# Kernel tuning notes

Hardware: AMD Instinct MI355X
Metric: run time of the kernel (lower is better)

Reference implementation:

```python
import jax, jax.numpy as jnp
import numpy as np

B, N, F, K = 16384, 64, 128, 64


def setup_inputs() -> dict:
    key = jax.random.key(0)
    kx, kd = jax.random.split(key)
    x = jax.random.normal(kx, (B, F), dtype=jnp.float32)
    D = jax.random.normal(kd, (N, F, K), dtype=jnp.float32)  # per-cluster factor dictionaries
    return {"x": x, "D": D}


def reference(x, D):
    # --- assignment step (torch.no_grad in original) ---
    # Dtx[n,b,j] = sum_i D[n,i,j] * x[b,i]
    Dtx = jnp.einsum('nij,bi->nbj', D, x)                      # [N,B,K]
    # per-cluster (D^T D)^{-1}, batched inverse over the cluster axis
    DTD = jnp.einsum('nij,nik->njk', D, D)                     # [N,K,K]
    DTD_inv = jnp.linalg.inv(DTD)                              # [N,K,K]
    Cs = jnp.einsum('nbj,nkj->nbk', Dtx, DTD_inv)              # [N,B,K]
    x_hat = jnp.einsum('nij,nbj->nbi', D, Cs)                  # [N,B,F]
    # nearest-subspace assignment per sample
    label = jnp.argmin(jnp.linalg.norm(x_hat - x[None], axis=-1), axis=0)  # [B] int
    C = Cs[label, jnp.arange(x.shape[0])]                      # [B,K] gather per sample
    # --- reconstruction loss: sum_i || x[i] - D[label[i]] @ C[i] ||^2 ---
    x_rec = jnp.einsum('bik,bk->bi', D[label], C)              # grouped gather + matmul
    se_loss = jnp.sum(jnp.square(x - x_rec))
    return se_loss, label
```

## Files before the change

kernel.cpp:

```cpp
#include <hip/hip_runtime.h>
#include <hip/hip_bf16.h>

#define B_N 16384
#define TAU 0.25f
#define GS 68
#define YS 133

typedef float f32x4 __attribute__((ext_vector_type(4)));
typedef short s16x8 __attribute__((ext_vector_type(8)));

__device__ __forceinline__ void gl_lds16(const void* g, void* l) {
    __builtin_amdgcn_global_load_lds(
        (const __attribute__((address_space(1))) void*)g,
        (__attribute__((address_space(3))) void*)l, 16, 0, 0);
}

__device__ __forceinline__ unsigned short bf16_bits(float v) {
    __hip_bfloat16 h = __float2bfloat16(v);
    return *reinterpret_cast<unsigned short*>(&h);
}

__device__ __forceinline__ float readlane_f(float v, int l) {
    return __int_as_float(__builtin_amdgcn_readlane(__float_as_int(v), l));
}

__global__ __launch_bounds__(256) void prep_convert(const float* __restrict__ x,
                                                    const float* __restrict__ D,
                                                    unsigned short* __restrict__ xh,
                                                    float* __restrict__ nrm,
                                                    float* __restrict__ Qg,
                                                    unsigned short* __restrict__ Bht,
                                                    float* __restrict__ out) {
    const int t = threadIdx.x;

    if (blockIdx.x >= 64) {
        const int gid = (blockIdx.x - 64) * 256 + t;
        if (gid == 0) out[0] = 0.0f;
        const size_t base = (size_t)gid * 32;
        float s = 0.0f;
        #pragma unroll
        for (int c = 0; c < 8; ++c) {
            const f32x4 v = ((const f32x4*)(x + base))[c];
            s += v.x * v.x + v.y * v.y + v.z * v.z + v.w * v.w;
            ushort4 h;
            h.x = bf16_bits(v.x); h.y = bf16_bits(v.y);
            h.z = bf16_bits(v.z); h.w = bf16_bits(v.w);
            ((ushort4*)(xh + base))[c] = h;
        }
        s += __shfl_xor(s, 1, 64);
        s += __shfl_xor(s, 2, 64);
        if ((gid & 3) == 0) nrm[gid >> 2] = s;
        return;
    }

    __shared__ float Y[64 * YS];
    __shared__ __align__(16) float G[64 * GS + 64];
    __shared__ __align__(16) float Lti[8 * 8 * 8];
    const int n = blockIdx.x;
    const float* Dn = D + (size_t)n * 8192;

    for (int e4 = t; e4 < 2048; e4 += 256) {
        const int c = e4 >> 4, j4 = (e4 & 15) * 4;
        const f32x4 v = ((const f32x4*)Dn)[e4];
        Y[(j4 + 0) * YS + c] = v.x;
        Y[(j4 + 1) * YS + c] = v.y;
        Y[(j4 + 2) * YS + c] = v.z;
        Y[(j4 + 3) * YS + c] = v.w;
    }

    {
        const int a0 = (t & 15) * 4, b0 = (t >> 4) * 4;
        float acc[4][4] = {};
        #pragma unroll 4
        for (int i = 0; i < 128; ++i) {
            const f32x4 av = *(const f32x4*)(Dn + i * 64 + a0);
            const f32x4 bv = *(const f32x4*)(Dn + i * 64 + b0);
            const float aa[4] = {av.x, av.y, av.z, av.w};
            const float bb[4] = {bv.x, bv.y, bv.z, bv.w};
            #pragma unroll
            for (int p = 0; p < 4; ++p)
                #pragma unroll
                for (int q = 0; q < 4; ++q) acc[p][q] = fmaf(aa[p], bb[q], acc[p][q]);
        }
        #pragma unroll
        for (int p = 0; p < 4; ++p)
            #pragma unroll
            for (int q = 0; q < 4; ++q) G[(a0 + p) * GS + b0 + q] = acc[p][q];
    }
    __syncthreads();

    #pragma unroll
    for (int p8 = 0; p8 < 8; ++p8) {
        const int pb = p8 * 8;
        if (t < 64) {
            const int lane = t;
            const f32x4 v0 = *(const f32x4*)&G[lane * GS + pb];
            const f32x4 v1 = *(const f32x4*)&G[lane * GS + pb + 4];
            float g[8] = {v0.x, v0.y, v0.z, v0.w, v1.x, v1.y, v1.z, v1.w};
            #pragma unroll
            for (int kk = 0; kk < 8; ++kk) {
                const int k = pb + kk;
                const float dk = readlane_f(g[kk], k);
                const float rinv = 1.0f / sqrtf(dk);
                const float lik = g[kk] * rinv;
                g[kk] = lik;
                if (lane == 0) G[64 * GS + k] = rinv;
                #pragma unroll
                for (int jj = kk + 1; jj < 8; ++jj) {
                    const float ljk = readlane_f(lik, pb + jj);
                    g[jj] -= lik * ljk;
                }
            }
            *(f32x4*)&G[lane * GS + pb]     = (f32x4){g[0], g[1], g[2], g[3]};
            *(f32x4*)&G[lane * GS + pb + 4] = (f32x4){g[4], g[5], g[6], g[7]};
        }
        __syncthreads();
        const int base = pb + 8;
        if (base < 64) {
            for (int i = base + (t >> 5); i < 64; i += 8) {
                const f32x4 Li0 = *(const f32x4*)&G[i * GS + pb];
                const f32x4 Li1 = *(const f32x4*)&G[i * GS + pb + 4];
                for (int j = base + (t & 31); j < 64; j += 32) {
                    const f32x4 Lj0 = *(const f32x4*)&G[j * GS + pb];
                    const f32x4 Lj1 = *(const f32x4*)&G[j * GS + pb + 4];
                    float s = G[i * GS + j];
                    s -= Li0.x * Lj0.x + Li0.y * Lj0.y + Li0.z * Lj0.z + Li0.w * Lj0.w;
                    s -= Li1.x * Lj1.x + Li1.y * Lj1.y + Li1.z * Lj1.z + Li1.w * Lj1.w;
                    G[i * GS + j] = s;
                }
            }
        }
        __syncthreads();
    }

    if (t < 64) {
        const int bi = t >> 3, c = t & 7;
        const int base = bi * 8;
        float m[8];
        #pragma unroll
        for (int r = 0; r < 8; ++r) {
            float s = (r == c) ? 1.0f : 0.0f;
            #pragma unroll
            for (int k = 0; k < r; ++k)
                s -= G[(base + r) * GS + base + k] * m[k];
            m[r] = s * G[64 * GS + base + r];
        }
        #pragma unroll
        for (int r = 0; r < 8; ++r) Lti[(base + r) * 8 + c] = m[r];
    }
    __syncthreads();

    if (t < 128) {
        const int c = t;
        for (int i = 0; i < 8; ++i) {
            float Tv[8];
            #pragma unroll
            for (int r = 0; r < 8; ++r) Tv[r] = Y[(i * 8 + r) * YS + c];
            for (int k = 0; k < i; ++k) {
                #pragma unroll
                for (int kk = 0; kk < 8; ++kk) {
                    const float z = Y[(k * 8 + kk) * YS + c];
                    #pragma unroll
                    for (int r = 0; r < 8; ++r)
                        Tv[r] -= G[(i * 8 + r) * GS + k * 8 + kk] * z;
                }
            }
            #pragma unroll
            for (int r = 0; r < 8; ++r) {
                float z = 0.0f;
                #pragma unroll
                for (int rp = 0; rp <= r; ++rp)
                    z += Lti[(i * 8 + r) * 8 + rp] * Tv[rp];
                Y[(i * 8 + r) * YS + c] = z;
            }
        }
    }
    __syncthreads();

    for (int e = t; e < 8192; e += 256) {
        const int j = e >> 7, i = e & 127;
        Bht[((size_t)n * 64 + j) * 128 + i] = bf16_bits(Y[j * YS + i]);
    }
    for (int e = t; e < 8192; e += 256) {
        const int i = e >> 6, j = e & 63;
        Qg[(size_t)n * 8192 + e] = Y[j * YS + i];
    }
}

__global__ __launch_bounds__(512) void gemm_argmax(const unsigned short* __restrict__ xh,
                                                   const unsigned short* __restrict__ Bht,
                                                   const float* __restrict__ nrm,
                                                   const float* __restrict__ x,
                                                   const float* __restrict__ Qg,
                                                   float* __restrict__ out) {
    __shared__ __align__(16) unsigned short ldsA[64 * 128];
    __shared__ float scL[64 * 65];
    __shared__ float mrg[8][64][3];
    __shared__ int sflags[64];
    __shared__ int scnt;
    __shared__ float ssum;
    __shared__ float scorr[8];

    const int t = threadIdx.x, w = t >> 6, lane = t & 63;
    const int m0 = blockIdx.x * 64;
    const int lm = lane & 15, lg = lane >> 4;
    if (t == 0) scnt = 0;
    if (t < 8) scorr[t] = 0.0f;

    {
        const int rl = lane >> 4, sp = lane & 15;
        #pragma unroll
        for (int q = 0; q < 2; ++q) {
            const int row = w * 8 + q * 4 + rl;
            const int c = sp ^ (row & 15);
            gl_lds16(xh + (size_t)(m0 + row) * 128 + c * 8,
                     &ldsA[(w * 8 + q * 4) * 128]);
        }
    }
    __syncthreads();

    s16x8 bfr[4][4];
    #pragma unroll
    for (int st = 0; st < 4; ++st) {
        const int r = st * 16 + lm;
        #pragma unroll
        for (int ks = 0; ks < 4; ++ks) {
            const int p = (ks * 4 + lg) ^ (r & 15);
            bfr[st][ks] = *(const s16x8*)&ldsA[r * 128 + p * 8];
        }
    }

    float v1[4] = {-1e30f, -1e30f, -1e30f, -1e30f};
    float v2[4] = {-1e30f, -1e30f, -1e30f, -1e30f};
    int   n1[4] = {0, 0, 0, 0};

    const unsigned short* afbase = Bht + (size_t)lm * 128 + lg * 8;

#define LOAD_AF(dst, cc) do {                                                   \
    const unsigned short* bp = afbase + (size_t)(cc) * 8192;                    \
    _Pragma("unroll")                                                           \
    for (int mt_ = 0; mt_ < 4; ++mt_)                                           \
        _Pragma("unroll")                                                       \
        for (int ks_ = 0; ks_ < 4; ++ks_)                                       \
            dst[mt_][ks_] = *(const s16x8*)(bp + mt_ * 2048 + ks_ * 32);        \
} while (0)

#define PROC(af, cc) do {                                                       \
    _Pragma("unroll")                                                           \
    for (int st_ = 0; st_ < 4; ++st_) {                                         \
        f32x4 ac0 = {0.f,0.f,0.f,0.f}, ac1 = {0.f,0.f,0.f,0.f};                 \
        f32x4 ac2 = {0.f,0.f,0.f,0.f}, ac3 = {0.f,0.f,0.f,0.f};                 \
        __builtin_amdgcn_s_setprio(1);                                          \
        _Pragma("unroll")                                                       \
        for (int ks_ = 0; ks_ < 4; ++ks_) {                                     \
            ac0 = __builtin_amdgcn_mfma_f32_16x16x32_bf16(af[0][ks_], bfr[st_][ks_], ac0, 0, 0, 0); \
            ac1 = __builtin_amdgcn_mfma_f32_16x16x32_bf16(af[1][ks_], bfr[st_][ks_], ac1, 0, 0, 0); \
            ac2 = __builtin_amdgcn_mfma_f32_16x16x32_bf16(af[2][ks_], bfr[st_][ks_], ac2, 0, 0, 0); \
            ac3 = __builtin_amdgcn_mfma_f32_16x16x32_bf16(af[3][ks_], bfr[st_][ks_], ac3, 0, 0, 0); \
        }                                                                       \
        __builtin_amdgcn_s_setprio(0);                                          \
        float q0 = ac0[0]*ac0[0]; q0 = fmaf(ac0[1],ac0[1],q0);                  \
        q0 = fmaf(ac0[2],ac0[2],q0); q0 = fmaf(ac0[3],ac0[3],q0);               \
        float q1 = ac1[0]*ac1[0]; q1 = fmaf(ac1[1],ac1[1],q1);                  \
        q1 = fmaf(ac1[2],ac1[2],q1); q1 = fmaf(ac1[3],ac1[3],q1);               \
        float q2 = ac2[0]*ac2[0]; q2 = fmaf(ac2[1],ac2[1],q2);                  \
        q2 = fmaf(ac2[2],ac2[2],q2); q2 = fmaf(ac2[3],ac2[3],q2);               \
        float q3 = ac3[0]*ac3[0]; q3 = fmaf(ac3[1],ac3[1],q3);                  \
        q3 = fmaf(ac3[2],ac3[2],q3); q3 = fmaf(ac3[3],ac3[3],q3);               \
        float s_ = ((q0 + q1) + q2) + q3;                                       \
        s_ += __shfl_xor(s_, 16, 64);                                           \
        s_ += __shfl_xor(s_, 32, 64);                                           \
        if (lg == 0) scL[(st_ * 16 + lm) * 65 + (cc)] = s_;                     \
        if (s_ > v1[st_]) { v2[st_] = v1[st_]; v1[st_] = s_; n1[st_] = (cc); }  \
        else v2[st_] = fmaxf(v2[st_], s_);                                      \
    }                                                                           \
} while (0)

    {
        const int cb = w * 8;
        s16x8 afA[4][4], afB[4][4];
        LOAD_AF(afA, cb);
        #pragma unroll 1
        for (int ci = 0; ci < 8; ci += 2) {
            LOAD_AF(afB, cb + ci + 1);
            PROC(afA, cb + ci);
            if (ci < 6) LOAD_AF(afA, cb + ci + 2);
            PROC(afB, cb + ci + 1);
        }
    }
#undef LOAD_AF
#undef PROC

    if (lg == 0) {
        #pragma unroll
        for (int st = 0; st < 4; ++st) {
            mrg[w][st * 16 + lm][0] = v1[st];
            mrg[w][st * 16 + lm][1] = v2[st];
            mrg[w][st * 16 + lm][2] = (float)n1[st];
        }
    }
    __syncthreads();

    if (t < 64) {
        float b1 = -1e30f, b2 = -1e30f;
        int bn = 0;
        #pragma unroll
        for (int ww = 0; ww < 8; ++ww) {
            const float a1 = mrg[ww][t][0];
            const float a2 = mrg[ww][t][1];
            const int an = (int)mrg[ww][t][2];
            if (a1 > b1) { b2 = fmaxf(b1, a2); b1 = a1; bn = an; }
            else b2 = fmaxf(b2, a1);
        }
        out[1 + m0 + t] = (float)bn;
        if (b1 - b2 < TAU) { const int i = atomicAdd(&scnt, 1); sflags[i] = t; }
        float err = nrm[m0 + t] - b1;
        err += __shfl_xor(err, 1, 64);
        err += __shfl_xor(err, 2, 64);
        err += __shfl_xor(err, 4, 64);
        err += __shfl_xor(err, 8, 64);
        err += __shfl_xor(err, 16, 64);
        err += __shfl_xor(err, 32, 64);
        if (t == 0) ssum = err;
    }
    __syncthreads();

    const int nf = scnt;
    float corr = 0.0f;
    for (int f = w; f < nf; f += 8) {
        const int s = sflags[f];
        const int b2 = m0 + s;
        const float v = scL[s * 65 + lane];
        float vm = v;
        for (int off = 32; off; off >>= 1) vm = fmaxf(vm, __shfl_xor(vm, off, 64));
        unsigned long long mask = __ballot((vm - v) < TAU);
        float best = -1e30f;
        int bn = 0;
        while (mask) {
            const int nn = (int)__builtin_ctzll(mask);
            mask &= mask - 1;
            const float* Qn = Qg + (size_t)nn * 8192;
            const float* xb = x + (size_t)b2 * 128;
            float d0 = 0.0f, d1 = 0.0f, d2 = 0.0f, d3 = 0.0f;
            #pragma unroll
            for (int i = 0; i < 128; i += 4) {
                d0 = fmaf(Qn[(i + 0) * 64 + lane], xb[i + 0], d0);
                d1 = fmaf(Qn[(i + 1) * 64 + lane], xb[i + 1], d1);
                d2 = fmaf(Qn[(i + 2) * 64 + lane], xb[i + 2], d2);
                d3 = fmaf(Qn[(i + 3) * 64 + lane], xb[i + 3], d3);
            }
            const float dot = (d0 + d1) + (d2 + d3);
            float sv = dot * dot;
            for (int off = 32; off; off >>= 1) sv += __shfl_xor(sv, off, 64);
            if (sv > best) { best = sv; bn = nn; }
        }
        if (lane == 0) {
            out[1 + b2] = (float)bn;
            corr += vm - best;
        }
    }
    if (lane == 0 && corr != 0.0f) scorr[w] += corr;
    __syncthreads();
    if (t == 0)
        atomicAdd(out, ssum + scorr[0] + scorr[1] + scorr[2] + scorr[3]
                       + scorr[4] + scorr[5] + scorr[6] + scorr[7]);
}

extern "C" void kernel_launch(void* const* d_in, const int* in_sizes, int n_in,
                              void* d_out, int out_size, void* d_ws, size_t ws_size,
                              hipStream_t stream) {
    const float* x = (const float*)d_in[0];
    const float* D = (const float*)d_in[1];
    float* out = (float*)d_out;

    char* ws = (char*)d_ws;
    unsigned short* xh  = (unsigned short*)(ws);
    unsigned short* Bht = (unsigned short*)(ws + (4u << 20));
    float* Qg           = (float*)(ws + (5u << 20));
    float* nrm          = (float*)(ws + (11u << 20));

    prep_convert<<<320, 256, 0, stream>>>(x, D, xh, nrm, Qg, Bht, out);
    gemm_argmax<<<256, 512, 0, stream>>>(xh, Bht, nrm, x, Qg, out);
}
```

Baseline: 143.4 us.

## Fuse prep and GEMM-argmax kernels into one cooperative kernel with grid sync

The separate factorization/convert kernel and the GEMM-argmax kernel are merged into a single cooperative launch of 256 blocks of 512 threads. A grid-wide barrier separates the phases. Shared memory is now a union buffer reused by both phases. This removes one kernel launch and the gap between launches, in exchange for cooperative-launch overhead, a grid sync, and prep blocks that run half their threads idle.

```diff
diff --git a/kernel.cpp b/kernel.cpp
--- a/kernel.cpp
+++ b/kernel.cpp
@@ -1,5 +1,8 @@
 #include <hip/hip_runtime.h>
 #include <hip/hip_bf16.h>
+#include <hip/hip_cooperative_groups.h>
+
+namespace cg = cooperative_groups;
 
 #define B_N 16384
 #define TAU 0.25f
@@ -24,17 +27,158 @@
     return __int_as_float(__builtin_amdgcn_readlane(__float_as_int(v), l));
 }
 
-__global__ __launch_bounds__(256) void prep_convert(const float* __restrict__ x,
-                                                    const float* __restrict__ D,
-                                                    unsigned short* __restrict__ xh,
-                                                    float* __restrict__ nrm,
-                                                    float* __restrict__ Qg,
-                                                    unsigned short* __restrict__ Bht,
-                                                    float* __restrict__ out) {
+__global__ __launch_bounds__(512) void fused_kfactor(const float* __restrict__ x,
+                                                     const float* __restrict__ D,
+                                                     unsigned short* __restrict__ xh,
+                                                     float* __restrict__ nrm,
+                                                     float* __restrict__ Qg,
+                                                     unsigned short* __restrict__ Bht,
+                                                     float* __restrict__ out) {
+    __shared__ __align__(16) unsigned char smem[53760];
+    __shared__ int sflags[64];
+    __shared__ int scnt;
+    __shared__ float ssum;
+    __shared__ float scorr[8];
+
     const int t = threadIdx.x;
-
-    if (blockIdx.x >= 64) {
-        const int gid = (blockIdx.x - 64) * 256 + t;
+    const int b = blockIdx.x;
+
+    if (b < 64) {
+        float* Y   = (float*)smem;
+        float* G   = (float*)(smem + 34048);
+        float* Lti = (float*)(smem + 51712);
+        const int n = b;
+        const float* Dn = D + (size_t)n * 8192;
+
+        if (t < 256) {
+            for (int e4 = t; e4 < 2048; e4 += 256) {
+                const int c = e4 >> 4, j4 = (e4 & 15) * 4;
+                const f32x4 v = ((const f32x4*)Dn)[e4];
+                Y[(j4 + 0) * YS + c] = v.x;
+                Y[(j4 + 1) * YS + c] = v.y;
+                Y[(j4 + 2) * YS + c] = v.z;
+                Y[(j4 + 3) * YS + c] = v.w;
+            }
+            const int a0 = (t & 15) * 4, b0 = (t >> 4) * 4;
+            float acc[4][4] = {};
+            #pragma unroll 4
+            for (int i = 0; i < 128; ++i) {
+                const f32x4 av = *(const f32x4*)(Dn + i * 64 + a0);
+                const f32x4 bv = *(const f32x4*)(Dn + i * 64 + b0);
+                const float aa[4] = {av.x, av.y, av.z, av.w};
+                const float bb[4] = {bv.x, bv.y, bv.z, bv.w};
+                #pragma unroll
+                for (int p = 0; p < 4; ++p)
+                    #pragma unroll
+                    for (int q = 0; q < 4; ++q) acc[p][q] = fmaf(aa[p], bb[q], acc[p][q]);
+            }
+            #pragma unroll
+            for (int p = 0; p < 4; ++p)
+                #pragma unroll
+                for (int q = 0; q < 4; ++q) G[(a0 + p) * GS + b0 + q] = acc[p][q];
+        }
+        __syncthreads();
+
+        #pragma unroll
+        for (int p8 = 0; p8 < 8; ++p8) {
+            const int pb = p8 * 8;
+            if (t < 64) {
+                const int lane = t;
+                const f32x4 v0 = *(const f32x4*)&G[lane * GS + pb];
+                const f32x4 v1 = *(const f32x4*)&G[lane * GS + pb + 4];
+                float g[8] = {v0.x, v0.y, v0.z, v0.w, v1.x, v1.y, v1.z, v1.w};
+                #pragma unroll
+                for (int kk = 0; kk < 8; ++kk) {
+                    const int k = pb + kk;
+                    const float dk = readlane_f(g[kk], k);
+                    const float rinv = 1.0f / sqrtf(dk);
+                    const float lik = g[kk] * rinv;
+                    g[kk] = lik;
+                    if (lane == 0) G[64 * GS + k] = rinv;
+                    #pragma unroll
+                    for (int jj = kk + 1; jj < 8; ++jj) {
+                        const float ljk = readlane_f(lik, pb + jj);
+                        g[jj] -= lik * ljk;
+                    }
+                }
+                *(f32x4*)&G[lane * GS + pb]     = (f32x4){g[0], g[1], g[2], g[3]};
+                *(f32x4*)&G[lane * GS + pb + 4] = (f32x4){g[4], g[5], g[6], g[7]};
+            }
+            __syncthreads();
+            const int base = pb + 8;
+            if (base < 64 && t < 256) {
+                for (int i = base + (t >> 5); i < 64; i += 8) {
+                    const f32x4 Li0 = *(const f32x4*)&G[i * GS + pb];
+                    const f32x4 Li1 = *(const f32x4*)&G[i * GS + pb + 4];
+                    for (int j = base + (t & 31); j < 64; j += 32) {
+                        const f32x4 Lj0 = *(const f32x4*)&G[j * GS + pb];
+                        const f32x4 Lj1 = *(const f32x4*)&G[j * GS + pb + 4];
+                        float s = G[i * GS + j];
+                        s -= Li0.x * Lj0.x + Li0.y * Lj0.y + Li0.z * Lj0.z + Li0.w * Lj0.w;
+                        s -= Li1.x * Lj1.x + Li1.y * Lj1.y + Li1.z * Lj1.z + Li1.w * Lj1.w;
+                        G[i * GS + j] = s;
+                    }
+                }
+            }
+            __syncthreads();
+        }
+
+        if (t < 64) {
+            const int bi = t >> 3, c = t & 7;
+            const int base = bi * 8;
+            float m[8];
+            #pragma unroll
+            for (int r = 0; r < 8; ++r) {
+                float s = (r == c) ? 1.0f : 0.0f;
+                #pragma unroll
+                for (int k = 0; k < r; ++k)
+                    s -= G[(base + r) * GS + base + k] * m[k];
+                m[r] = s * G[64 * GS + base + r];
+            }
+            #pragma unroll
+            for (int r = 0; r < 8; ++r) Lti[(base + r) * 8 + c] = m[r];
+        }
+        __syncthreads();
+
+        if (t < 128) {
+            const int c = t;
+            for (int i = 0; i < 8; ++i) {
+                float Tv[8];
+                #pragma unroll
+                for (int r = 0; r < 8; ++r) Tv[r] = Y[(i * 8 + r) * YS + c];
+                for (int k = 0; k < i; ++k) {
+                    #pragma unroll
+                    for (int kk = 0; kk < 8; ++kk) {
+                        const float z = Y[(k * 8 + kk) * YS + c];
+                        #pragma unroll
+                        for (int r = 0; r < 8; ++r)
+                            Tv[r] -= G[(i * 8 + r) * GS + k * 8 + kk] * z;
+                    }
+                }
+                #pragma unroll
+                for (int r = 0; r < 8; ++r) {
+                    float z = 0.0f;
+                    #pragma unroll
+                    for (int rp = 0; rp <= r; ++rp)
+                        z += Lti[(i * 8 + r) * 8 + rp] * Tv[rp];
+                    Y[(i * 8 + r) * YS + c] = z;
+                }
+            }
+        }
+        __syncthreads();
+
+        if (t < 256) {
+            for (int e = t; e < 8192; e += 256) {
+                const int j = e >> 7, i = e & 127;
+                Bht[((size_t)n * 64 + j) * 128 + i] = bf16_bits(Y[j * YS + i]);
+            }
+            for (int e = t; e < 8192; e += 256) {
+                const int i = e >> 6, j = e & 63;
+                Qg[(size_t)n * 8192 + e] = Y[j * YS + i];
+            }
+        }
+    } else if (b < 192) {
+        const int gid = (b - 64) * 512 + t;
         if (gid == 0) out[0] = 0.0f;
         const size_t base = (size_t)gid * 32;
         float s = 0.0f;
@@ -50,159 +194,15 @@
         s += __shfl_xor(s, 1, 64);
         s += __shfl_xor(s, 2, 64);
         if ((gid & 3) == 0) nrm[gid >> 2] = s;
-        return;
-    }
-
-    __shared__ float Y[64 * YS];
-    __shared__ __align__(16) float G[64 * GS + 64];
-    __shared__ __align__(16) float Lti[8 * 8 * 8];
-    const int n = blockIdx.x;
-    const float* Dn = D + (size_t)n * 8192;
-
-    for (int e4 = t; e4 < 2048; e4 += 256) {
-        const int c = e4 >> 4, j4 = (e4 & 15) * 4;
-        const f32x4 v = ((const f32x4*)Dn)[e4];
-        Y[(j4 + 0) * YS + c] = v.x;
-        Y[(j4 + 1) * YS + c] = v.y;
-        Y[(j4 + 2) * YS + c] = v.z;
-        Y[(j4 + 3) * YS + c] = v.w;
-    }
-
-    {
-        const int a0 = (t & 15) * 4, b0 = (t >> 4) * 4;
-        float acc[4][4] = {};
-        #pragma unroll 4
-        for (int i = 0; i < 128; ++i) {
-            const f32x4 av = *(const f32x4*)(Dn + i * 64 + a0);
-            const f32x4 bv = *(const f32x4*)(Dn + i * 64 + b0);
-            const float aa[4] = {av.x, av.y, av.z, av.w};
-            const float bb[4] = {bv.x, bv.y, bv.z, bv.w};
-            #pragma unroll
-            for (int p = 0; p < 4; ++p)
-                #pragma unroll
-                for (int q = 0; q < 4; ++q) acc[p][q] = fmaf(aa[p], bb[q], acc[p][q]);
-        }
-        #pragma unroll
-        for (int p = 0; p < 4; ++p)
-            #pragma unroll
-            for (int q = 0; q < 4; ++q) G[(a0 + p) * GS + b0 + q] = acc[p][q];
-    }
-    __syncthreads();
-
-    #pragma unroll
-    for (int p8 = 0; p8 < 8; ++p8) {
-        const int pb = p8 * 8;
-        if (t < 64) {
-            const int lane = t;
-            const f32x4 v0 = *(const f32x4*)&G[lane * GS + pb];
-            const f32x4 v1 = *(const f32x4*)&G[lane * GS + pb + 4];
-            float g[8] = {v0.x, v0.y, v0.z, v0.w, v1.x, v1.y, v1.z, v1.w};
-            #pragma unroll
-            for (int kk = 0; kk < 8; ++kk) {
-                const int k = pb + kk;
-                const float dk = readlane_f(g[kk], k);
-                const float rinv = 1.0f / sqrtf(dk);
-                const float lik = g[kk] * rinv;
-                g[kk] = lik;
-                if (lane == 0) G[64 * GS + k] = rinv;
-                #pragma unroll
-                for (int jj = kk + 1; jj < 8; ++jj) {
-                    const float ljk = readlane_f(lik, pb + jj);
-                    g[jj] -= lik * ljk;
-                }
-            }
-            *(f32x4*)&G[lane * GS + pb]     = (f32x4){g[0], g[1], g[2], g[3]};
-            *(f32x4*)&G[lane * GS + pb + 4] = (f32x4){g[4], g[5], g[6], g[7]};
-        }
-        __syncthreads();
-        const int base = pb + 8;
-        if (base < 64) {
-            for (int i = base + (t >> 5); i < 64; i += 8) {
-                const f32x4 Li0 = *(const f32x4*)&G[i * GS + pb];
-                const f32x4 Li1 = *(const f32x4*)&G[i * GS + pb + 4];
-                for (int j = base + (t & 31); j < 64; j += 32) {
-                    const f32x4 Lj0 = *(const f32x4*)&G[j * GS + pb];
-                    const f32x4 Lj1 = *(const f32x4*)&G[j * GS + pb + 4];
-                    float s = G[i * GS + j];
-                    s -= Li0.x * Lj0.x + Li0.y * Lj0.y + Li0.z * Lj0.z + Li0.w * Lj0.w;
-                    s -= Li1.x * Lj1.x + Li1.y * Lj1.y + Li1.z * Lj1.z + Li1.w * Lj1.w;
-                    G[i * GS + j] = s;
-                }
-            }
-        }
-        __syncthreads();
-    }
-
-    if (t < 64) {
-        const int bi = t >> 3, c = t & 7;
-        const int base = bi * 8;
-        float m[8];
-        #pragma unroll
-        for (int r = 0; r < 8; ++r) {
-            float s = (r == c) ? 1.0f : 0.0f;
-            #pragma unroll
-            for (int k = 0; k < r; ++k)
-                s -= G[(base + r) * GS + base + k] * m[k];
-            m[r] = s * G[64 * GS + base + r];
-        }
-        #pragma unroll
-        for (int r = 0; r < 8; ++r) Lti[(base + r) * 8 + c] = m[r];
-    }
-    __syncthreads();
-
-    if (t < 128) {
-        const int c = t;
-        for (int i = 0; i < 8; ++i) {
-            float Tv[8];
-            #pragma unroll
-            for (int r = 0; r < 8; ++r) Tv[r] = Y[(i * 8 + r) * YS + c];
-            for (int k = 0; k < i; ++k) {
-                #pragma unroll
-                for (int kk = 0; kk < 8; ++kk) {
-                    const float z = Y[(k * 8 + kk) * YS + c];
-                    #pragma unroll
-                    for (int r = 0; r < 8; ++r)
-                        Tv[r] -= G[(i * 8 + r) * GS + k * 8 + kk] * z;
-                }
-            }
-            #pragma unroll
-            for (int r = 0; r < 8; ++r) {
-                float z = 0.0f;
-                #pragma unroll
-                for (int rp = 0; rp <= r; ++rp)
-                    z += Lti[(i * 8 + r) * 8 + rp] * Tv[rp];
-                Y[(i * 8 + r) * YS + c] = z;
-            }
-        }
-    }
-    __syncthreads();
-
-    for (int e = t; e < 8192; e += 256) {
-        const int j = e >> 7, i = e & 127;
-        Bht[((size_t)n * 64 + j) * 128 + i] = bf16_bits(Y[j * YS + i]);
-    }
-    for (int e = t; e < 8192; e += 256) {
-        const int i = e >> 6, j = e & 63;
-        Qg[(size_t)n * 8192 + e] = Y[j * YS + i];
-    }
-}
-
-__global__ __launch_bounds__(512) void gemm_argmax(const unsigned short* __restrict__ xh,
-                                                   const unsigned short* __restrict__ Bht,
-                                                   const float* __restrict__ nrm,
-                                                   const float* __restrict__ x,
-                                                   const float* __restrict__ Qg,
-                                                   float* __restrict__ out) {
-    __shared__ __align__(16) unsigned short ldsA[64 * 128];
-    __shared__ float scL[64 * 65];
-    __shared__ float mrg[8][64][3];
-    __shared__ int sflags[64];
-    __shared__ int scnt;
-    __shared__ float ssum;
-    __shared__ float scorr[8];
-
-    const int t = threadIdx.x, w = t >> 6, lane = t & 63;
-    const int m0 = blockIdx.x * 64;
+    }
+
+    cg::this_grid().sync();
+
+    unsigned short* ldsA = (unsigned short*)smem;
+    float* scL = (float*)(smem + 16384);
+    float* mrg = (float*)(smem + 33024);
+    const int w = t >> 6, lane = t & 63;
+    const int m0 = b * 64;
     const int lm = lane & 15, lg = lane >> 4;
     if (t == 0) scnt = 0;
     if (t < 8) scorr[t] = 0.0f;
@@ -294,9 +294,9 @@
     if (lg == 0) {
         #pragma unroll
         for (int st = 0; st < 4; ++st) {
-            mrg[w][st * 16 + lm][0] = v1[st];
-            mrg[w][st * 16 + lm][1] = v2[st];
-            mrg[w][st * 16 + lm][2] = (float)n1[st];
+            mrg[(w * 64 + st * 16 + lm) * 3 + 0] = v1[st];
+            mrg[(w * 64 + st * 16 + lm) * 3 + 1] = v2[st];
+            mrg[(w * 64 + st * 16 + lm) * 3 + 2] = (float)n1[st];
         }
     }
     __syncthreads();
@@ -306,9 +306,9 @@
         int bn = 0;
         #pragma unroll
         for (int ww = 0; ww < 8; ++ww) {
-            const float a1 = mrg[ww][t][0];
-            const float a2 = mrg[ww][t][1];
-            const int an = (int)mrg[ww][t][2];
+            const float a1 = mrg[(ww * 64 + t) * 3 + 0];
+            const float a2 = mrg[(ww * 64 + t) * 3 + 1];
+            const int an = (int)mrg[(ww * 64 + t) * 3 + 2];
             if (a1 > b1) { b2 = fmaxf(b1, a2); b1 = a1; bn = an; }
             else b2 = fmaxf(b2, a1);
         }
@@ -379,6 +379,8 @@
     float* Qg           = (float*)(ws + (5u << 20));
     float* nrm          = (float*)(ws + (11u << 20));
 
-    prep_convert<<<320, 256, 0, stream>>>(x, D, xh, nrm, Qg, Bht, out);
-    gemm_argmax<<<256, 512, 0, stream>>>(xh, Bht, nrm, x, Qg, out);
-}
+    void* args[] = {(void*)&x, (void*)&D, (void*)&xh, (void*)&nrm,
+                    (void*)&Qg, (void*)&Bht, (void*)&out};
+    hipLaunchCooperativeKernel((const void*)fused_kfactor,
+                               dim3(256), dim3(512), args, 0, stream);
+}
```

Result: slower. 187.4 us (+30.6%).
